# Kernel optimization log

Hardware: AMD Instinct MI355X
Metric: run time of the kernel (lower is better)

The kernel has to match this reference:

```python
import jax, jax.numpy as jnp
import numpy as np

NUM_HEADS = 16


def setup_inputs() -> dict:
    key = jax.random.key(0)
    ks = jax.random.split(key, 5)
    B, L, H = 2, 2048, 2048
    scale = 1.0 / np.sqrt(H)
    return {
        "x": jax.random.normal(ks[0], (B, L, H), dtype=jnp.float32),
        "padding_mask": jnp.zeros((B, L), dtype=bool),  # True = padded/masked
        "Wq": jax.random.normal(ks[1], (H, H), dtype=jnp.float32) * scale,
        "Wk": jax.random.normal(ks[2], (H, H), dtype=jnp.float32) * scale,
        "Wv": jax.random.normal(ks[3], (H, H), dtype=jnp.float32) * scale,
        "Wo": jax.random.normal(ks[4], (H, H), dtype=jnp.float32) * scale,
    }


def reference(x, padding_mask, Wq, Wk, Wv, Wo):
    B, L, H = x.shape
    nh = NUM_HEADS
    dh = H // nh

    def proj(W):  # torch Linear (no bias): x @ W.T, then split heads -> (B, nh, L, dh)
        return jnp.einsum('blh,oh->blo', x, W).reshape(B, L, nh, dh).transpose(0, 2, 1, 3)

    q, k, v = proj(Wq), proj(Wk), proj(Wv)

    # scores (B, nh, L, L) = Q K^T / sqrt(d_head)
    scores = jnp.einsum('bhqd,bhkd->bhqk', q, k) / jnp.sqrt(jnp.asarray(dh, x.dtype))

    causal = jnp.triu(jnp.ones((L, L), dtype=bool), k=1)          # True above diagonal = masked
    mask = causal[None, None, :, :] | padding_mask[:, None, None, :]
    masked_scores = jnp.where(mask, -jnp.inf, scores)

    attn = jax.nn.softmax(masked_scores, axis=-1)                  # (B, nh, L, L)
    mixed = jnp.einsum('bhqk,bhkd->bhqd', attn, v)                 # (B, nh, L, dh)
    merged = mixed.transpose(0, 2, 1, 3).reshape(B, L, H)
    out = jnp.einsum('blh,oh->blo', merged, Wo)
    return out
```

## Files before the change

kernel.cpp:

```cpp
#include <hip/hip_runtime.h>


#define DEVI __device__ __forceinline__

typedef __attribute__((ext_vector_type(4))) float f32x4;
typedef __attribute__((ext_vector_type(16))) float f32x16;
typedef __attribute__((ext_vector_type(8))) short short8;
typedef __attribute__((ext_vector_type(8))) __bf16 bf16x8;
typedef __attribute__((ext_vector_type(4))) unsigned short us4;
typedef __attribute__((ext_vector_type(4))) unsigned int u32x4;

typedef __attribute__((address_space(1))) void* gas1p;
typedef __attribute__((address_space(3))) void* las3p;

static constexpr int Lq = 2048;
static constexpr int DH = 128;
static constexpr float QSCALE = 0.08838834764831845f * 1.4426950408889634f;

DEVI f32x4 mfma16(short8 a, short8 b, f32x4 c) {
  return __builtin_amdgcn_mfma_f32_16x16x32_bf16(
      __builtin_bit_cast(bf16x8, a), __builtin_bit_cast(bf16x8, b), c, 0, 0, 0);
}

DEVI f32x16 mfma32(short8 a, short8 b, f32x16 c) {
  return __builtin_amdgcn_mfma_f32_32x32x16_bf16(
      __builtin_bit_cast(bf16x8, a), __builtin_bit_cast(bf16x8, b), c, 0, 0, 0);
}

DEVI unsigned short f2bf(float f) {
  union { float f; unsigned u; } v; v.f = f;
  return (unsigned short)((v.u + 0x7fffu + ((v.u >> 16) & 1u)) >> 16);
}

DEVI float fexp2(float x) {
  float r;
  asm("v_exp_f32 %0, %1" : "=v"(r) : "v"(x));
  return r;
}

DEVI unsigned cvtpk(float lo, float hi) {
  unsigned r;
  asm("v_cvt_pk_bf16_f32 %0, %1, %2" : "=v"(r) : "v"(lo), "v"(hi));
  return r;
}

DEVI void plswap(unsigned& a, unsigned& b) {
  auto r = __builtin_amdgcn_permlane32_swap(a, b, false, false);
  a = r[0]; b = r[1];
}

DEVI float xmax32(float x) {
  unsigned a = __builtin_bit_cast(unsigned, x), b = a;
  plswap(a, b);
  return fmaxf(__builtin_bit_cast(float, a), __builtin_bit_cast(float, b));
}
DEVI float xadd32(float x) {
  unsigned a = __builtin_bit_cast(unsigned, x), b = a;
  plswap(a, b);
  return __builtin_bit_cast(float, a) + __builtin_bit_cast(float, b);
}

__global__ __launch_bounds__(256) void cvt_all(
    const float* __restrict__ x, const float* __restrict__ wq,
    const float* __restrict__ wk, const float* __restrict__ wv,
    const float* __restrict__ wo, unsigned short* __restrict__ d) {
  const int i = blockIdx.x * 256 + threadIdx.x;
  const float* s;
  size_t si, di;
  if (i < 2097152) {
    s = x; si = i; di = i;
  } else {
    const int j = i - 2097152;
    const int sel = j >> 20;
    const int off = j & 1048575;
    s = (sel == 0) ? wq : (sel == 1) ? wk : (sel == 2) ? wv : wo;
    si = off;
    di = 2097152 + (size_t)sel * 1048576 + off;
  }
  f32x4 v = *(const f32x4*)(s + si * 4);
  us4 o;
  o.x = f2bf(v.x); o.y = f2bf(v.y); o.z = f2bf(v.z); o.w = f2bf(v.w);
  *(us4*)(d + di * 4) = o;
}

template <int MODE>
__global__ __launch_bounds__(512, 2) void gemm256(
    const unsigned short* __restrict__ A, const unsigned short* __restrict__ Bw,
    void* __restrict__ C0, void* __restrict__ C1, void* __restrict__ C2,
    int M, int N, int K, int gx_log2, int nwg) {
  __shared__ __align__(16) char lds[131072];
  const int tid = threadIdx.x;
  const int lane = tid & 63;
  const int w = tid >> 6;
  const int g = lane >> 4, c = lane & 15;
  const int wm = w >> 2, wn = w & 3;

  const int lin = blockIdx.x;
  const int wg = (lin & 7) * (nwg >> 3) + (lin >> 3);
  const int m0 = (wg & ((1 << gx_log2) - 1)) * 256;
  const int n0 = (wg >> gx_log2) * 256;

  const char* Ab = (const char*)A;
  const char* Bb = (const char*)Bw;
  const size_t K2 = (size_t)K * 2;

  const int slotw = ((c & 1) * 4 + g) ^ ((c >> 1) & 7);
  const int aoff = (wm * 64 + (c >> 1)) * 128 + slotw * 16;
  const int boff = 16384 + (wn * 32 + (c >> 1)) * 128 + slotw * 16;

  f32x4 acc[8][4] = {};

#define STG(BUF, S)                                                            \
  do {                                                                         \
    const size_t kob = (size_t)(S) * 64;                                       \
    _Pragma("unroll") for (int it = 0; it < 2; ++it) {                         \
      const int ch = it * 512 + tid;                                           \
      const int sr = ch >> 3, sl = ch & 7;                                     \
      const int ll = sl ^ (sr & 7);                                            \
      const size_t rowa = (size_t)(m0 + sr * 2 + (ll >> 2));                   \
      __builtin_amdgcn_global_load_lds(                                        \
          (gas1p)(void*)(Ab + rowa * K2 + kob + (ll & 3) * 16),                \
          (las3p)(lds + (BUF) * 32768 + ch * 16), 16, 0, 0);                   \
      const size_t rowb = (size_t)(n0 + sr * 2 + (ll >> 2));                   \
      __builtin_amdgcn_global_load_lds(                                        \
          (gas1p)(void*)(Bb + rowb * K2 + kob + (ll & 3) * 16),                \
          (las3p)(lds + (BUF) * 32768 + 16384 + ch * 16), 16, 0, 0);           \
    }                                                                          \
  } while (0)

#define FRAGS_MFMA(BC)                                                         \
  do {                                                                         \
    const char* bufc = lds + (BC) * 32768;                                     \
    short8 af[8], bf[4];                                                       \
    _Pragma("unroll") for (int m = 0; m < 8; ++m)                              \
        af[m] = *(const short8*)(bufc + aoff + m * 1024);                      \
    _Pragma("unroll") for (int n = 0; n < 4; ++n)                              \
        bf[n] = *(const short8*)(bufc + boff + n * 1024);                      \
    __builtin_amdgcn_s_setprio(1);                                             \
    _Pragma("unroll") for (int m = 0; m < 8; ++m)                              \
        _Pragma("unroll") for (int n = 0; n < 4; ++n)                          \
        acc[m][n] = mfma16(af[m], bf[n], acc[m][n]);                           \
    __builtin_amdgcn_s_setprio(0);                                             \
  } while (0)

#define BAR() asm volatile("s_barrier" ::: "memory")
#define WVM(N) asm volatile("s_waitcnt vmcnt(" #N ")" ::: "memory")

#define PHASE(BC, BS, S, VM)                                                   \
  do {                                                                         \
    STG(BS, S);                                                                \
    FRAGS_MFMA(BC);                                                            \
    WVM(VM);                                                                   \
    BAR();                                                                     \
  } while (0)

  STG(0, 0);
  STG(1, 1);
  STG(2, 2);
  WVM(8);
  BAR();

  for (int s = 0; s < 60; s += 4) {
    PHASE(0, 3, s + 3, 8);
    PHASE(1, 0, s + 4, 8);
    PHASE(2, 1, s + 5, 8);
    PHASE(3, 2, s + 6, 8);
  }
  PHASE(0, 3, 63, 8);
  FRAGS_MFMA(1); WVM(4); BAR();
  FRAGS_MFMA(2); WVM(0); BAR();
  FRAGS_MFMA(3);

#undef PHASE
#undef WVM
#undef BAR
#undef FRAGS_MFMA
#undef STG

  const int region = (MODE == 4) ? (n0 >> 11) : 0;
#pragma unroll
  for (int m = 0; m < 8; ++m) {
#pragma unroll
    for (int n = 0; n < 4; ++n) {
      const int col = n0 + wn * 64 + n * 16 + c;
#pragma unroll
      for (int r = 0; r < 4; ++r) {
        const int row = m0 + wm * 128 + m * 16 + g * 4 + r;
        const float v = acc[m][n][r];
        if (MODE == 2) {
          ((float*)C0)[(size_t)row * N + col] = v;
        } else {
          const int b = row >> 11, l = row & 2047;
          const int cc = col & 2047;
          const int h = cc >> 7, dd = cc & 127;
          if (region == 0) {
            ((unsigned short*)C0)[(((size_t)(b * 16 + h) * 2048 + l) << 7) + dd] =
                f2bf(v * QSCALE);
          } else if (region == 1) {
            ((unsigned short*)C1)[(((size_t)(b * 16 + h) * 2048 + l) << 7) + dd] =
                f2bf(v);
          } else {
            ((unsigned short*)C2)[(((size_t)(b * 16 + h) * 128 + dd) << 11) + l] =
                f2bf(v);
          }
        }
      }
    }
  }
}

__global__ __launch_bounds__(256) void attn_causal(
    const unsigned short* __restrict__ Q, const unsigned short* __restrict__ K,
    const unsigned short* __restrict__ VT, unsigned short* __restrict__ O) {
  __shared__ __align__(16) char smem[65536];
  char* Ks0 = smem;
  char* Vs0 = smem + 16384;
  char* Ks1 = smem + 32768;
  char* Vs1 = smem + 49152;

  const int tid = threadIdx.x;
  const int lane = tid & 63, w = tid >> 6;
  const int l31 = lane & 31, hi = lane >> 5;
  const int hi4 = hi * 4;
  const int swz = (l31 & 7) << 4;
  const int lin = blockIdx.x;
  const int xcd = lin & 7;
  const int slot = lin >> 3;
  const int qt_raw = slot & 15;
  const int qt = ((slot >> 5) & 1) ? qt_raw : 15 - qt_raw;
  const int bh = (slot >> 4) * 8 + xcd;
  const int q0 = qt * 128;
  const int q_base = q0 + w * 32;
  const int q_lane = q_base + l31;

  const char* Qb = (const char*)(Q + (size_t)bh * Lq * DH);
  const char* Kb = (const char*)(K + (size_t)bh * Lq * DH);
  const char* Vb = (const char*)(VT + (size_t)bh * DH * Lq);

  short8 qf[8];
#pragma unroll
  for (int ch = 0; ch < 8; ++ch)
    qf[ch] = *(const short8*)(Qb + (size_t)q_lane * 256 + ch * 32 + hi * 16);

  f32x16 o[4] = {};
  float mr = -__builtin_inff(), lr = 0.f;

  const int ntiles = 2 * qt + 2;

#define STAGE(KS, VS, T)                                                       \
  do {                                                                         \
    const size_t kb0 = (size_t)(T) * 64 * 256;                                 \
    const size_t vb0 = (size_t)(T) * 128;                                      \
    _Pragma("unroll") for (int it = 0; it < 4; ++it) {                         \
      const int chunk = it * 256 + tid;                                        \
      const int krow = chunk >> 4, kcb = (chunk & 15) * 16;                    \
      __builtin_amdgcn_global_load_lds(                                        \
          (gas1p)(void*)(Kb + kb0 + (size_t)krow * 256 +                       \
                         (kcb ^ ((krow & 7) << 4))),                           \
          (las3p)((KS) + chunk * 16), 16, 0, 0);                               \
      const int vd = chunk >> 3, vcb = (chunk & 7) * 16;                       \
      __builtin_amdgcn_global_load_lds(                                        \
          (gas1p)(void*)(Vb + (size_t)vd * 4096 + vb0 +                        \
                         (vcb ^ ((vd & 7) << 4))),                             \
          (las3p)((VS) + chunk * 16), 16, 0, 0);                               \
    }                                                                          \
  } while (0)

#define COMPUTE(KS, VS, T)                                                     \
  do {                                                                         \
    const int kv0 = (T) * 64;                                                  \
    if (kv0 <= q_base + 31) {                                                  \
      f32x16 s0 = {}, s1 = {};                                                 \
      __builtin_amdgcn_s_setprio(1);                                           \
      _Pragma("unroll") for (int ch = 0; ch < 8; ++ch) {                       \
        const short8 kf0 = *(const short8*)((KS) + l31 * 256 +                 \
                                            ((ch * 32 + hi * 16) ^ swz));      \
        const short8 kf1 = *(const short8*)((KS) + (32 + l31) * 256 +          \
                                            ((ch * 32 + hi * 16) ^ swz));      \
        s0 = mfma32(kf0, qf[ch], s0);                                          \
        s1 = mfma32(kf1, qf[ch], s1);                                          \
      }                                                                        \
      __builtin_amdgcn_s_setprio(0);                                           \
      float vv[32];                                                            \
      _Pragma("unroll") for (int r = 0; r < 16; ++r) {                         \
        vv[r] = s0[r];                                                         \
        vv[16 + r] = s1[r];                                                    \
      }                                                                        \
      if (kv0 + 63 > q_base) {                                                 \
        _Pragma("unroll") for (int st = 0; st < 2; ++st)                       \
            _Pragma("unroll") for (int r = 0; r < 16; ++r) {                   \
          const int kv = kv0 + st * 32 + (r & 3) + 8 * (r >> 2) + hi4;         \
          if (kv > q_lane) vv[st * 16 + r] = -__builtin_inff();                \
        }                                                                      \
      }                                                                        \
      float t16[16];                                                           \
      _Pragma("unroll") for (int i = 0; i < 16; ++i)                           \
          t16[i] = fmaxf(vv[i], vv[i + 16]);                                   \
      _Pragma("unroll") for (int i = 0; i < 8; ++i)                            \
          t16[i] = fmaxf(t16[i], t16[i + 8]);                                  \
      _Pragma("unroll") for (int i = 0; i < 4; ++i)                            \
          t16[i] = fmaxf(t16[i], t16[i + 4]);                                  \
      const float mx =                                                         \
          xmax32(fmaxf(fmaxf(t16[0], t16[1]), fmaxf(t16[2], t16[3])));         \
      if (__any(mx - mr > 8.0f)) {      \
        const float mn = fmaxf(mr, mx);                                        \
        const float al = fexp2(mr - mn);                                       \
        mr = mn;                                                               \
        lr *= al;                                                              \
        _Pragma("unroll") for (int dt = 0; dt < 4; ++dt)                       \
            _Pragma("unroll") for (int r = 0; r < 16; ++r) o[dt][r] *= al;     \
      }                                                                        \
      _Pragma("unroll") for (int i = 0; i < 32; ++i)                           \
          vv[i] = fexp2(vv[i] - mr);                                           \
      _Pragma("unroll") for (int i = 0; i < 16; ++i)                           \
          t16[i] = vv[i] + vv[i + 16];                                         \
      _Pragma("unroll") for (int i = 0; i < 8; ++i)                            \
          t16[i] = t16[i] + t16[i + 8];                                        \
      _Pragma("unroll") for (int i = 0; i < 4; ++i)                            \
          t16[i] = t16[i] + t16[i + 4];                                        \
      lr += xadd32((t16[0] + t16[1]) + (t16[2] + t16[3]));                     \
      short8 pfr[4];                                                           \
      _Pragma("unroll") for (int ks = 0; ks < 4; ++ks) {                       \
        unsigned A0 = cvtpk(vv[ks * 8 + 0], vv[ks * 8 + 1]);                   \
        unsigned A1 = cvtpk(vv[ks * 8 + 2], vv[ks * 8 + 3]);                   \
        unsigned B0 = cvtpk(vv[ks * 8 + 4], vv[ks * 8 + 5]);                   \
        unsigned B1 = cvtpk(vv[ks * 8 + 6], vv[ks * 8 + 7]);                   \
        plswap(A0, B0);                                                        \
        plswap(A1, B1);                                                        \
        u32x4 fw;                                                              \
        fw.x = A0; fw.y = A1; fw.z = B0; fw.w = B1;                            \
        pfr[ks] = __builtin_bit_cast(short8, fw);                              \
      }                                                                        \
      __builtin_amdgcn_s_setprio(1);                                           \
      _Pragma("unroll") for (int dt = 0; dt < 4; ++dt)                         \
          _Pragma("unroll") for (int ks = 0; ks < 4; ++ks) {                   \
        const short8 vf = *(const short8*)((VS) + (dt * 32 + l31) * 128 +      \
                                           ((ks * 32 + hi * 16) ^ swz));       \
        o[dt] = mfma32(vf, pfr[ks], o[dt]);                                    \
      }                                                                        \
      __builtin_amdgcn_s_setprio(0);                                           \
    }                                                                          \
  } while (0)

  STAGE(Ks0, Vs0, 0);
  asm volatile("s_waitcnt vmcnt(0)" ::: "memory");
  __builtin_amdgcn_s_barrier();

  int t = 0;
  for (;;) {
    if (t + 1 < ntiles) STAGE(Ks1, Vs1, t + 1);
    COMPUTE(Ks0, Vs0, t);
    asm volatile("s_waitcnt vmcnt(0)" ::: "memory");
    __builtin_amdgcn_s_barrier();
    if (++t >= ntiles) break;
    if (t + 1 < ntiles) STAGE(Ks0, Vs0, t + 1);
    COMPUTE(Ks1, Vs1, t);
    asm volatile("s_waitcnt vmcnt(0)" ::: "memory");
    __builtin_amdgcn_s_barrier();
    if (++t >= ntiles) break;
  }
#undef STAGE
#undef COMPUTE

  __syncthreads();
  {
    char* buf = smem + w * 16384;
    const float invl = 1.0f / lr;
#pragma unroll
    for (int dt = 0; dt < 4; ++dt)
#pragma unroll
      for (int r = 0; r < 16; ++r) {
        const int d = dt * 32 + (r & 3) + 8 * (r >> 2) + hi4;
        *(unsigned short*)(buf + l31 * 256 + ((d * 2) ^ swz)) =
            f2bf(o[dt][r] * invl);
      }
    const int b = bh >> 4, h = bh & 15;
#pragma unroll
    for (int i = 0; i < 8; ++i) {
      const int cidx = i * 64 + lane;
      const int q = cidx >> 4, chk = cidx & 15;
      const short8 vvv =
          *(const short8*)(buf + q * 256 + ((chk * 16) ^ ((q & 7) << 4)));
      *(short8*)(O + ((size_t)(b * Lq + q0 + w * 32 + q)) * 2048 + h * 128 +
                 chk * 8) = vvv;
    }
  }
}

extern "C" void kernel_launch(void* const* d_in, const int* in_sizes, int n_in,
                              void* d_out, int out_size, void* d_ws, size_t ws_size,
                              hipStream_t stream) {
  (void)in_sizes; (void)n_in; (void)out_size; (void)ws_size;
  const float* x = (const float*)d_in[0];
  const float* wq = (const float*)d_in[2];
  const float* wk = (const float*)d_in[3];
  const float* wv = (const float*)d_in[4];
  const float* wo = (const float*)d_in[5];

  unsigned short* ws = (unsigned short*)d_ws;
  unsigned short* xb  = ws;
  unsigned short* wqb = ws + 8388608;
  unsigned short* wob = ws + 20971520;
  unsigned short* qb  = ws + 25165824;
  unsigned short* kb  = ws + 33554432;
  unsigned short* vtb = ws + 41943040;
  unsigned short* ob  = ws + 50331648;

  cvt_all<<<24576, 256, 0, stream>>>(x, wq, wk, wv, wo, ws);

  gemm256<4><<<dim3(384), 512, 0, stream>>>(xb, wqb, qb, kb, vtb,
                                            4096, 6144, 2048, 4, 384);
  attn_causal<<<dim3(512), 256, 0, stream>>>(qb, kb, vtb, ob);
  gemm256<2><<<dim3(128), 512, 0, stream>>>(ob, wob, d_out, nullptr, nullptr,
                                            4096, 2048, 2048, 4, 128);
}
```

Baseline: 323.9 us.

## Restructure GEMM mainloop into half-tile ping-pong staging with K=64 steps

The 256x256 bf16 GEMM main loop moves from a 4-buffer K=32 pipeline to a 2-buffer K=64 layout with separate A and B regions, staged in half-tiles. Each of four sub-phases reads A fragments for two M-frags while keeping the B fragments in registers, issues one half-tile global-to-LDS load, then synchronises with a barrier before the MFMAs. The aim is finer-grained interleaving of loads and MFMA, with fewer LDS reads per MFMA. In exchange it adds more barriers per K step and holds more live registers for B fragments.

```diff
diff --git a/kernel.cpp b/kernel.cpp
--- a/kernel.cpp
+++ b/kernel.cpp
@@ -84,7 +84,7 @@
 }
 
 template <int MODE>
-__global__ __launch_bounds__(512, 2) void gemm256(
+__global__ __launch_bounds__(512, 2) void gemm256p(
     const unsigned short* __restrict__ A, const unsigned short* __restrict__ Bw,
     void* __restrict__ C0, void* __restrict__ C1, void* __restrict__ C2,
     int M, int N, int K, int gx_log2, int nwg) {
@@ -104,78 +104,110 @@
   const char* Bb = (const char*)Bw;
   const size_t K2 = (size_t)K * 2;
 
-  const int slotw = ((c & 1) * 4 + g) ^ ((c >> 1) & 7);
-  const int aoff = (wm * 64 + (c >> 1)) * 128 + slotw * 16;
-  const int boff = 16384 + (wn * 32 + (c >> 1)) * 128 + slotw * 16;
+  const int arow = wm * 128 + c;
+  const int brow = wn * 64 + c;
+  const int sK0 = (g ^ (c & 7)) * 16;
+  const int sK1 = ((4 + g) ^ (c & 7)) * 16;
 
   f32x4 acc[8][4] = {};
-
-#define STG(BUF, S)                                                            \
+  short8 bfr[4][2];
+
+#define STGH(ISB, H, T)                                                        \
   do {                                                                         \
-    const size_t kob = (size_t)(S) * 64;                                       \
+    const int p_ = (T) & 1;                                                    \
+    const size_t kb_ = (size_t)(T) * 128;                                      \
     _Pragma("unroll") for (int it = 0; it < 2; ++it) {                         \
       const int ch = it * 512 + tid;                                           \
-      const int sr = ch >> 3, sl = ch & 7;                                     \
-      const int ll = sl ^ (sr & 7);                                            \
-      const size_t rowa = (size_t)(m0 + sr * 2 + (ll >> 2));                   \
+      const int r_ = (H) * 128 + (ch >> 3);                                    \
+      const int sl_ = ch & 7;                                                  \
+      const int ll_ = sl_ ^ (r_ & 7);                                          \
+      const size_t grow_ = (size_t)(((ISB) ? n0 : m0) + r_);                   \
       __builtin_amdgcn_global_load_lds(                                        \
-          (gas1p)(void*)(Ab + rowa * K2 + kob + (ll & 3) * 16),                \
-          (las3p)(lds + (BUF) * 32768 + ch * 16), 16, 0, 0);                   \
-      const size_t rowb = (size_t)(n0 + sr * 2 + (ll >> 2));                   \
-      __builtin_amdgcn_global_load_lds(                                        \
-          (gas1p)(void*)(Bb + rowb * K2 + kob + (ll & 3) * 16),                \
-          (las3p)(lds + (BUF) * 32768 + 16384 + ch * 16), 16, 0, 0);           \
+          (gas1p)(void*)(((ISB) ? Bb : Ab) + grow_ * K2 + kb_ + ll_ * 16),     \
+          (las3p)(lds + ((ISB) ? 65536 : 0) + p_ * 32768 + r_ * 128 +          \
+                  sl_ * 16),                                                   \
+          16, 0, 0);                                                           \
     }                                                                          \
   } while (0)
 
-#define FRAGS_MFMA(BC)                                                         \
-  do {                                                                         \
-    const char* bufc = lds + (BC) * 32768;                                     \
-    short8 af[8], bf[4];                                                       \
-    _Pragma("unroll") for (int m = 0; m < 8; ++m)                              \
-        af[m] = *(const short8*)(bufc + aoff + m * 1024);                      \
-    _Pragma("unroll") for (int n = 0; n < 4; ++n)                              \
-        bf[n] = *(const short8*)(bufc + boff + n * 1024);                      \
-    __builtin_amdgcn_s_setprio(1);                                             \
-    _Pragma("unroll") for (int m = 0; m < 8; ++m)                              \
-        _Pragma("unroll") for (int n = 0; n < 4; ++n)                          \
-        acc[m][n] = mfma16(af[m], bf[n], acc[m][n]);                           \
-    __builtin_amdgcn_s_setprio(0);                                             \
-  } while (0)
-
 #define BAR() asm volatile("s_barrier" ::: "memory")
 #define WVM(N) asm volatile("s_waitcnt vmcnt(" #N ")" ::: "memory")
-
-#define PHASE(BC, BS, S, VM)                                                   \
+#define LGKM0() asm volatile("s_waitcnt lgkmcnt(0)" ::: "memory")
+
+#define RD_A(DST, P, MF, SK)                                                   \
+  DST = *(const short8*)(lds + (P) * 32768 + (arow + (MF) * 16) * 128 + (SK))
+#define RD_B(DST, P, NF, SK)                                                   \
+  DST = *(const short8*)(lds + 65536 + (P) * 32768 + (brow + (NF) * 16) * 128 +\
+                         (SK))
+
+#define PH_A(P, Q, STG_STMT, TAILW)                                            \
   do {                                                                         \
-    STG(BS, S);                                                                \
-    FRAGS_MFMA(BC);                                                            \
-    WVM(VM);                                                                   \
+    short8 a00, a01, a10, a11;                                                 \
+    RD_A(a00, P, 2 * (Q), sK0);                                                \
+    RD_A(a01, P, 2 * (Q), sK1);                                                \
+    RD_A(a10, P, 2 * (Q) + 1, sK0);                                            \
+    RD_A(a11, P, 2 * (Q) + 1, sK1);                                            \
+    STG_STMT;                                                                  \
+    BAR();                                                                     \
+    LGKM0();                                                                   \
+    __builtin_amdgcn_s_setprio(1);                                             \
+    _Pragma("unroll") for (int nf = 0; nf < 4; ++nf) {                         \
+      acc[2 * (Q)][nf] = mfma16(a00, bfr[nf][0], acc[2 * (Q)][nf]);            \
+      acc[2 * (Q)][nf] = mfma16(a01, bfr[nf][1], acc[2 * (Q)][nf]);            \
+      acc[2 * (Q) + 1][nf] = mfma16(a10, bfr[nf][0], acc[2 * (Q) + 1][nf]);    \
+      acc[2 * (Q) + 1][nf] = mfma16(a11, bfr[nf][1], acc[2 * (Q) + 1][nf]);    \
+    }                                                                          \
+    __builtin_amdgcn_s_setprio(0);                                             \
+    TAILW;                                                                     \
     BAR();                                                                     \
   } while (0)
 
-  STG(0, 0);
-  STG(1, 1);
-  STG(2, 2);
-  WVM(8);
+#define LOAD_BFR(P)                                                            \
+  do {                                                                         \
+    _Pragma("unroll") for (int nf = 0; nf < 4; ++nf) {                         \
+      RD_B(bfr[nf][0], P, nf, sK0);                                            \
+      RD_B(bfr[nf][1], P, nf, sK1);                                            \
+    }                                                                          \
+  } while (0)
+
+  STGH(1, 0, 0); STGH(1, 1, 0);
+  STGH(0, 0, 0); STGH(0, 1, 0);
+  STGH(1, 0, 1); STGH(1, 1, 1);
+  WVM(4);
   BAR();
 
-  for (int s = 0; s < 60; s += 4) {
-    PHASE(0, 3, s + 3, 8);
-    PHASE(1, 0, s + 4, 8);
-    PHASE(2, 1, s + 5, 8);
-    PHASE(3, 2, s + 6, 8);
+  for (int i = 0; i < 15; ++i) {
+    const int U = 2 * i;
+    LOAD_BFR(0);
+    PH_A(0, 0, STGH(0, 0, U + 1), (void)0);
+    PH_A(0, 1, STGH(0, 1, U + 1), (void)0);
+    PH_A(0, 2, STGH(1, 0, U + 2), (void)0);
+    PH_A(0, 3, STGH(1, 1, U + 2), WVM(4));
+    LOAD_BFR(1);
+    PH_A(1, 0, STGH(0, 0, U + 2), (void)0);
+    PH_A(1, 1, STGH(0, 1, U + 2), (void)0);
+    PH_A(1, 2, STGH(1, 0, U + 3), (void)0);
+    PH_A(1, 3, STGH(1, 1, U + 3), WVM(4));
   }
-  PHASE(0, 3, 63, 8);
-  FRAGS_MFMA(1); WVM(4); BAR();
-  FRAGS_MFMA(2); WVM(0); BAR();
-  FRAGS_MFMA(3);
-
-#undef PHASE
+  LOAD_BFR(0);
+  PH_A(0, 0, STGH(0, 0, 31), (void)0);
+  PH_A(0, 1, STGH(0, 1, 31), (void)0);
+  PH_A(0, 2, (void)0, (void)0);
+  PH_A(0, 3, (void)0, WVM(0));
+  LOAD_BFR(1);
+  PH_A(1, 0, (void)0, (void)0);
+  PH_A(1, 1, (void)0, (void)0);
+  PH_A(1, 2, (void)0, (void)0);
+  PH_A(1, 3, (void)0, (void)0);
+
+#undef LOAD_BFR
+#undef PH_A
+#undef RD_B
+#undef RD_A
+#undef LGKM0
 #undef WVM
 #undef BAR
-#undef FRAGS_MFMA
-#undef STG
+#undef STGH
 
   const int region = (MODE == 4) ? (n0 >> 11) : 0;
 #pragma unroll
@@ -408,9 +440,9 @@
 
   cvt_all<<<24576, 256, 0, stream>>>(x, wq, wk, wv, wo, ws);
 
-  gemm256<4><<<dim3(384), 512, 0, stream>>>(xb, wqb, qb, kb, vtb,
-                                            4096, 6144, 2048, 4, 384);
+  gemm256p<4><<<dim3(384), 512, 0, stream>>>(xb, wqb, qb, kb, vtb,
+                                             4096, 6144, 2048, 4, 384);
   attn_causal<<<dim3(512), 256, 0, stream>>>(qb, kb, vtb, ob);
-  gemm256<2><<<dim3(128), 512, 0, stream>>>(ob, wob, d_out, nullptr, nullptr,
-                                            4096, 2048, 2048, 4, 128);
-}
+  gemm256p<2><<<dim3(128), 512, 0, stream>>>(ob, wob, d_out, nullptr, nullptr,
+                                             4096, 2048, 2048, 4, 128);
+}
```

Measured after the change: 319.8 us. About the same (-1.3%).
